# Performance work log

Hardware: AMD Instinct MI355X
Metric: run time of the kernel (lower is better)

The kernel has to match this reference:

```python
import jax, jax.numpy as jnp
import numpy as np

N_NODES = 50000
N_EDGES = 800000
IN_FEATS = 128
OUT_FEATS = 128


def setup_inputs() -> dict:
    key = jax.random.key(0)
    k1, k2, k3, k4, k5 = jax.random.split(key, 5)
    # xavier_uniform for W
    limit = float(np.sqrt(6.0 / (IN_FEATS + OUT_FEATS)))
    W = jax.random.uniform(k2, (IN_FEATS, OUT_FEATS), jnp.float32, -limit, limit)
    return {
        "feat": jax.random.normal(k1, (N_NODES, IN_FEATS), jnp.float32),
        "W": W,
        "b": jnp.zeros((OUT_FEATS,), jnp.float32),
        "edge_w": jax.random.uniform(k3, (N_EDGES,), jnp.float32),
        "edge_src": jax.random.randint(k4, (N_EDGES,), 0, N_NODES),
        "edge_dst": jax.random.randint(k5, (N_EDGES,), 0, N_NODES),
    }


def reference(feat, W, b, edge_w, edge_src, edge_dst):
    N = feat.shape[0]
    ones = jnp.ones(edge_src.shape[0], feat.dtype)
    # norm == 'both': scale src features by out_degree^{-1/2}
    out_deg = jnp.clip(jax.ops.segment_sum(ones, edge_src, num_segments=N), 1.0)
    feat = feat * (out_deg ** -0.5)[:, None]  # [N, in]
    # in_feats (128) is NOT > out_feats (128): aggregate first, then matmul
    msgs = feat[edge_src] * edge_w[:, None]  # [E, in] (u_mul_e)
    agg = jax.ops.segment_sum(msgs, edge_dst, num_segments=N)  # [N, in] (sum)
    rst = agg @ W  # [N, out]
    # dst-side normalization: in_degree^{-1/2}
    in_deg = jnp.clip(jax.ops.segment_sum(ones, edge_dst, num_segments=N), 1.0)
    rst = rst * (in_deg ** -0.5)[:, None] + b
    return rst
```

## Files before the change

### kernel.cpp

```cpp
#include <hip/hip_runtime.h>
#include <math.h>

#define N_NODES 50000
#define N_EDGES 800000
#define F 128
#define CAP 64


__global__ __launch_bounds__(256) void hist_kernel(
    const int* __restrict__ src, int* __restrict__ out_deg) {
    int i = blockIdx.x * blockDim.x + threadIdx.x;
    if (i < N_EDGES) atomicAdd(&out_deg[src[i]], 1);
}

__global__ __launch_bounds__(256) void place_kernel(
    const int* __restrict__ src, const int* __restrict__ dst,
    const float* __restrict__ edge_w, const int* __restrict__ out_deg,
    int* __restrict__ cnt, int2* __restrict__ meta) {
    int e = blockIdx.x * blockDim.x + threadIdx.x;
    if (e >= N_EDGES) return;
    int s = src[e];
    int d = dst[e];
    float w = edge_w[e] * rsqrtf(fmaxf((float)out_deg[s], 1.0f));
    int pos = atomicAdd(&cnt[d], 1);
    if (pos < CAP)
        meta[(size_t)d * CAP + pos] = make_int2(s, __float_as_int(w));
}

__global__ __launch_bounds__(256) void gather_kernel(
    const float* __restrict__ feat, const int* __restrict__ cnt,
    const int2* __restrict__ meta, float* __restrict__ agg) {
    int wid = (blockIdx.x * blockDim.x + threadIdx.x) >> 6;
    if (wid >= N_NODES) return;
    int lane = threadIdx.x & 63;
    int half = lane >> 5, l = lane & 31;
    int c = cnt[wid];
    if (c > CAP) c = CAP;
    const int2* m = meta + (size_t)wid * CAP;
    float4 acc = make_float4(0.f, 0.f, 0.f, 0.f);
    int j = half;
    for (; j + 2 < c; j += 4) {
        int2 m0 = m[j];
        int2 m1 = m[j + 2];
        float w0 = __int_as_float(m0.y);
        float w1 = __int_as_float(m1.y);
        float4 v0 = ((const float4*)(feat + (size_t)m0.x * F))[l];
        float4 v1 = ((const float4*)(feat + (size_t)m1.x * F))[l];
        acc.x += w0 * v0.x; acc.y += w0 * v0.y;
        acc.z += w0 * v0.z; acc.w += w0 * v0.w;
        acc.x += w1 * v1.x; acc.y += w1 * v1.y;
        acc.z += w1 * v1.z; acc.w += w1 * v1.w;
    }
    for (; j < c; j += 2) {
        int2 m0 = m[j];
        float w0 = __int_as_float(m0.y);
        float4 v0 = ((const float4*)(feat + (size_t)m0.x * F))[l];
        acc.x += w0 * v0.x; acc.y += w0 * v0.y;
        acc.z += w0 * v0.z; acc.w += w0 * v0.w;
    }
    acc.x += __shfl_xor(acc.x, 32, 64);
    acc.y += __shfl_xor(acc.y, 32, 64);
    acc.z += __shfl_xor(acc.z, 32, 64);
    acc.w += __shfl_xor(acc.w, 32, 64);
    if (half == 0)
        ((float4*)(agg + (size_t)wid * F))[l] = acc;
}

__global__ __launch_bounds__(256) void gemm_inplace(
    const float* __restrict__ W, const float* __restrict__ bias,
    const int* __restrict__ cnt, float* __restrict__ io) {
    __shared__ float As[64][132];
    __shared__ float Ws[128][128];

    int tid = threadIdx.x;
    int row0 = blockIdx.x * 64;

    for (int q = tid; q < 64 * 32; q += 256) {
        int r = q >> 5, c4 = q & 31;
        int gr = row0 + r;
        float4 v = make_float4(0.f, 0.f, 0.f, 0.f);
        if (gr < N_NODES) v = ((const float4*)(io + (size_t)gr * F))[c4];
        *(float4*)&As[r][c4 * 4] = v;
    }
    for (int q = tid; q < 128 * 32; q += 256) {
        int r = q >> 5, c4 = q & 31;
        *(float4*)&Ws[r][c4 * 4] = ((const float4*)(W + r * F))[c4];
    }
    __syncthreads();

    int tx = tid & 15, ty = tid >> 4;
    float acc[4][8] = {{0.f}};
    for (int k = 0; k < F; ++k) {
        float a[4];
#pragma unroll
        for (int i = 0; i < 4; ++i) a[i] = As[ty * 4 + i][k];
        float4 b0 = *(float4*)&Ws[k][tx * 4];
        float4 b1 = *(float4*)&Ws[k][64 + tx * 4];
#pragma unroll
        for (int i = 0; i < 4; ++i) {
            acc[i][0] += a[i] * b0.x;
            acc[i][1] += a[i] * b0.y;
            acc[i][2] += a[i] * b0.z;
            acc[i][3] += a[i] * b0.w;
            acc[i][4] += a[i] * b1.x;
            acc[i][5] += a[i] * b1.y;
            acc[i][6] += a[i] * b1.z;
            acc[i][7] += a[i] * b1.w;
        }
    }

#pragma unroll
    for (int i = 0; i < 4; ++i) {
        int gr = row0 + ty * 4 + i;
        if (gr >= N_NODES) continue;
        float sc = rsqrtf(fmaxf((float)cnt[gr], 1.0f));
        float4 o0, o1;
        o0.x = acc[i][0] * sc + bias[tx * 4 + 0];
        o0.y = acc[i][1] * sc + bias[tx * 4 + 1];
        o0.z = acc[i][2] * sc + bias[tx * 4 + 2];
        o0.w = acc[i][3] * sc + bias[tx * 4 + 3];
        o1.x = acc[i][4] * sc + bias[64 + tx * 4 + 0];
        o1.y = acc[i][5] * sc + bias[64 + tx * 4 + 1];
        o1.z = acc[i][6] * sc + bias[64 + tx * 4 + 2];
        o1.w = acc[i][7] * sc + bias[64 + tx * 4 + 3];
        ((float4*)(io + (size_t)gr * F))[tx] = o0;
        ((float4*)(io + (size_t)gr * F))[16 + tx] = o1;
    }
}

extern "C" void kernel_launch(void* const* d_in, const int* in_sizes, int n_in,
                              void* d_out, int out_size, void* d_ws, size_t ws_size,
                              hipStream_t stream) {
    const float* feat   = (const float*)d_in[0];
    const float* W      = (const float*)d_in[1];
    const float* bias   = (const float*)d_in[2];
    const float* edge_w = (const float*)d_in[3];
    const int* edge_src = (const int*)d_in[4];
    const int* edge_dst = (const int*)d_in[5];
    float* out = (float*)d_out;

    int2* meta   = (int2*)d_ws;
    int* cnt     = (int*)((char*)d_ws + (size_t)N_NODES * CAP * sizeof(int2));
    int* out_deg = cnt + N_NODES;

    hipMemsetAsync(cnt, 0, (size_t)2 * N_NODES * sizeof(int), stream);

    hist_kernel<<<(N_EDGES + 255) / 256, 256, 0, stream>>>(edge_src, out_deg);

    place_kernel<<<(N_EDGES + 255) / 256, 256, 0, stream>>>(
        edge_src, edge_dst, edge_w, out_deg, cnt, meta);

    gather_kernel<<<(N_NODES * 64 + 255) / 256, 256, 0, stream>>>(
        feat, cnt, meta, out);

    gemm_inplace<<<(N_NODES + 63) / 64, 256, 0, stream>>>(
        W, bias, cnt, out);
}
```

Before: 275.3 us.

## Fuse out-degree histogram into placement and K-tile the GEMM shared memory

Drops the separate out-degree histogram kernel. The out-degree atomics now run inside the placement kernel, and the source normalisation is applied at gather time by reading out_deg for each edge. Separately, the in-place GEMM now loads A and W in 32-wide K tiles instead of staging the full 64x128 and 128x128 tiles, which cuts shared memory per block from about 97KB to about 25KB to allow higher occupancy. In exchange, the gather does an extra scattered out_deg load per edge, and the GEMM adds syncs per K tile.

```diff
diff --git a/kernel.cpp b/kernel.cpp
--- a/kernel.cpp
+++ b/kernel.cpp
@@ -7,29 +7,24 @@
 #define CAP 64
 
 
-__global__ __launch_bounds__(256) void hist_kernel(
-    const int* __restrict__ src, int* __restrict__ out_deg) {
-    int i = blockIdx.x * blockDim.x + threadIdx.x;
-    if (i < N_EDGES) atomicAdd(&out_deg[src[i]], 1);
-}
-
 __global__ __launch_bounds__(256) void place_kernel(
     const int* __restrict__ src, const int* __restrict__ dst,
-    const float* __restrict__ edge_w, const int* __restrict__ out_deg,
-    int* __restrict__ cnt, int2* __restrict__ meta) {
+    const float* __restrict__ edge_w,
+    int* __restrict__ out_deg, int* __restrict__ cnt, int2* __restrict__ meta) {
     int e = blockIdx.x * blockDim.x + threadIdx.x;
     if (e >= N_EDGES) return;
     int s = src[e];
     int d = dst[e];
-    float w = edge_w[e] * rsqrtf(fmaxf((float)out_deg[s], 1.0f));
+    atomicAdd(&out_deg[s], 1);
     int pos = atomicAdd(&cnt[d], 1);
     if (pos < CAP)
-        meta[(size_t)d * CAP + pos] = make_int2(s, __float_as_int(w));
+        meta[(size_t)d * CAP + pos] = make_int2(s, __float_as_int(edge_w[e]));
 }
 
 __global__ __launch_bounds__(256) void gather_kernel(
     const float* __restrict__ feat, const int* __restrict__ cnt,
-    const int2* __restrict__ meta, float* __restrict__ agg) {
+    const int* __restrict__ out_deg, const int2* __restrict__ meta,
+    float* __restrict__ agg) {
     int wid = (blockIdx.x * blockDim.x + threadIdx.x) >> 6;
     if (wid >= N_NODES) return;
     int lane = threadIdx.x & 63;
@@ -42,8 +37,8 @@
     for (; j + 2 < c; j += 4) {
         int2 m0 = m[j];
         int2 m1 = m[j + 2];
-        float w0 = __int_as_float(m0.y);
-        float w1 = __int_as_float(m1.y);
+        float w0 = __int_as_float(m0.y) * rsqrtf(fmaxf((float)out_deg[m0.x], 1.0f));
+        float w1 = __int_as_float(m1.y) * rsqrtf(fmaxf((float)out_deg[m1.x], 1.0f));
         float4 v0 = ((const float4*)(feat + (size_t)m0.x * F))[l];
         float4 v1 = ((const float4*)(feat + (size_t)m1.x * F))[l];
         acc.x += w0 * v0.x; acc.y += w0 * v0.y;
@@ -53,7 +48,7 @@
     }
     for (; j < c; j += 2) {
         int2 m0 = m[j];
-        float w0 = __int_as_float(m0.y);
+        float w0 = __int_as_float(m0.y) * rsqrtf(fmaxf((float)out_deg[m0.x], 1.0f));
         float4 v0 = ((const float4*)(feat + (size_t)m0.x * F))[l];
         acc.x += w0 * v0.x; acc.y += w0 * v0.y;
         acc.z += w0 * v0.z; acc.w += w0 * v0.w;
@@ -69,43 +64,51 @@
 __global__ __launch_bounds__(256) void gemm_inplace(
     const float* __restrict__ W, const float* __restrict__ bias,
     const int* __restrict__ cnt, float* __restrict__ io) {
-    __shared__ float As[64][132];
-    __shared__ float Ws[128][128];
+    __shared__ float As[64][36];
+    __shared__ float Ws[32][128];
 
     int tid = threadIdx.x;
     int row0 = blockIdx.x * 64;
+    int tx = tid & 15, ty = tid >> 4;
 
-    for (int q = tid; q < 64 * 32; q += 256) {
-        int r = q >> 5, c4 = q & 31;
-        int gr = row0 + r;
-        float4 v = make_float4(0.f, 0.f, 0.f, 0.f);
-        if (gr < N_NODES) v = ((const float4*)(io + (size_t)gr * F))[c4];
-        *(float4*)&As[r][c4 * 4] = v;
-    }
-    for (int q = tid; q < 128 * 32; q += 256) {
-        int r = q >> 5, c4 = q & 31;
-        *(float4*)&Ws[r][c4 * 4] = ((const float4*)(W + r * F))[c4];
-    }
-    __syncthreads();
-
-    int tx = tid & 15, ty = tid >> 4;
     float acc[4][8] = {{0.f}};
-    for (int k = 0; k < F; ++k) {
-        float a[4];
+    for (int kt = 0; kt < 4; ++kt) {
+        __syncthreads();
 #pragma unroll
-        for (int i = 0; i < 4; ++i) a[i] = As[ty * 4 + i][k];
-        float4 b0 = *(float4*)&Ws[k][tx * 4];
-        float4 b1 = *(float4*)&Ws[k][64 + tx * 4];
+        for (int p = 0; p < 2; ++p) {
+            int q = tid + p * 256;
+            int r = q >> 3, c4 = q & 7;
+            int gr = row0 + r;
+            float4 v = make_float4(0.f, 0.f, 0.f, 0.f);
+            if (gr < N_NODES)
+                v = ((const float4*)(io + (size_t)gr * F + kt * 32))[c4];
+            *(float4*)&As[r][c4 * 4] = v;
+        }
 #pragma unroll
-        for (int i = 0; i < 4; ++i) {
-            acc[i][0] += a[i] * b0.x;
-            acc[i][1] += a[i] * b0.y;
-            acc[i][2] += a[i] * b0.z;
-            acc[i][3] += a[i] * b0.w;
-            acc[i][4] += a[i] * b1.x;
-            acc[i][5] += a[i] * b1.y;
-            acc[i][6] += a[i] * b1.z;
-            acc[i][7] += a[i] * b1.w;
+        for (int p = 0; p < 4; ++p) {
+            int q = tid + p * 256;
+            int r = q >> 5, c4 = q & 31;
+            *(float4*)&Ws[r][c4 * 4] = ((const float4*)(W + (size_t)(kt * 32 + r) * F))[c4];
+        }
+        __syncthreads();
+#pragma unroll
+        for (int k = 0; k < 32; ++k) {
+            float a[4];
+#pragma unroll
+            for (int i = 0; i < 4; ++i) a[i] = As[ty * 4 + i][k];
+            float4 b0 = *(float4*)&Ws[k][tx * 4];
+            float4 b1 = *(float4*)&Ws[k][64 + tx * 4];
+#pragma unroll
+            for (int i = 0; i < 4; ++i) {
+                acc[i][0] += a[i] * b0.x;
+                acc[i][1] += a[i] * b0.y;
+                acc[i][2] += a[i] * b0.z;
+                acc[i][3] += a[i] * b0.w;
+                acc[i][4] += a[i] * b1.x;
+                acc[i][5] += a[i] * b1.y;
+                acc[i][6] += a[i] * b1.z;
+                acc[i][7] += a[i] * b1.w;
+            }
         }
     }
 
@@ -145,13 +148,11 @@
 
     hipMemsetAsync(cnt, 0, (size_t)2 * N_NODES * sizeof(int), stream);
 
-    hist_kernel<<<(N_EDGES + 255) / 256, 256, 0, stream>>>(edge_src, out_deg);
-
     place_kernel<<<(N_EDGES + 255) / 256, 256, 0, stream>>>(
         edge_src, edge_dst, edge_w, out_deg, cnt, meta);
 
     gather_kernel<<<(N_NODES * 64 + 255) / 256, 256, 0, stream>>>(
-        feat, cnt, meta, out);
+        feat, cnt, out_deg, meta, out);
 
     gemm_inplace<<<(N_NODES + 63) / 64, 256, 0, stream>>>(
         W, bias, cnt, out);
```

Result: faster. 249.7 us (-9.3%).
